# Optimization experiments

Measured on AMD Instinct MI355X. Metric: run time of the kernel, lower is better.

Reference implementation:

```python
import jax, jax.numpy as jnp
import numpy as np

VISION_TOKEN_TYPE = 1
HIDDEN = 4096
INTER = 11008


def setup_inputs() -> dict:
    key = jax.random.key(0)
    ks = jax.random.split(key, 8)
    B, L, D, F = 2, 2048, HIDDEN, INTER
    s_in = 1.0 / np.sqrt(D)
    s_mid = 1.0 / np.sqrt(F)
    inp = {
        "hidden_states": jax.random.normal(ks[0], (B, L, D), dtype=jnp.float32),
        "token_type_ids": jax.random.randint(ks[1], (B, L), 0, 2, dtype=jnp.int64),
        # language expert weights (stored as [in, out] for x @ W)
        "lang_gate": jax.random.normal(ks[2], (D, F), dtype=jnp.float32) * s_in,
        "lang_up": jax.random.normal(ks[3], (D, F), dtype=jnp.float32) * s_in,
        "lang_down": jax.random.normal(ks[4], (F, D), dtype=jnp.float32) * s_mid,
        # vision expert weights
        "vis_gate": jax.random.normal(ks[5], (D, F), dtype=jnp.float32) * s_in,
        "vis_up": jax.random.normal(ks[6], (D, F), dtype=jnp.float32) * s_in,
        "vis_down": jax.random.normal(ks[7], (F, D), dtype=jnp.float32) * s_mid,
    }
    return inp


def _swiglu_mlp(x, w_gate, w_up, w_down):
    # x: (B, L, D) -> (B, L, D)
    return (jax.nn.silu(x @ w_gate) * (x @ w_up)) @ w_down


def _vision_mask(token_type_ids):
    # vision token i is one whose type AND next token's type are VISION_TOKEN_TYPE;
    # last position is always language.
    is_vis = token_type_ids == VISION_TOKEN_TYPE
    pair = is_vis[:, :-1] & is_vis[:, 1:]
    return jnp.pad(pair, ((0, 0), (0, 1)), constant_values=False)  # (B, L) bool


def reference(hidden_states, token_type_ids, lang_gate, lang_up, lang_down,
              vis_gate, vis_up, vis_down):
    vision_mask = _vision_mask(token_type_ids)  # (B, L)
    out_vis = _swiglu_mlp(hidden_states, vis_gate, vis_up, vis_down)
    out_lang = _swiglu_mlp(hidden_states, lang_gate, lang_up, lang_down)
    return jnp.where(vision_mask[..., None], out_vis, out_lang)
```

## Files before the change

### kernel.cpp

```cpp
#include <hip/hip_runtime.h>
#include <cstdint>

#define HD 4096
#define FF 11008
#define BB 2
#define LL 2048
#define BL (BB*LL)
#define NM 16
#define NN 86

using bf16x8  = __attribute__((ext_vector_type(8))) __bf16;
using f32x4   = __attribute__((ext_vector_type(4))) float;
using ushort8 = __attribute__((ext_vector_type(8))) unsigned short;

__device__ __forceinline__ int imin(int a, int b) { return a < b ? a : b; }

__device__ __forceinline__ unsigned short f2bf(float f) {
  union { float f; unsigned u; } v; v.f = f;
  unsigned r = v.u + 0x7fffu + ((v.u >> 16) & 1u);
  return (unsigned short)(r >> 16);
}

__device__ __forceinline__ void gld_lds16(const void* g, void* l) {
  __builtin_amdgcn_global_load_lds(
      (__attribute__((address_space(1))) void*)g,
      (__attribute__((address_space(3))) void*)l, 16, 0, 0);
}

__global__ void detect_mode(const int* __restrict__ w, int* __restrict__ flag) {
  int acc = 0;
  for (int i = 1 + 2 * (int)threadIdx.x; i < BL; i += 512) acc |= w[i];
  if (acc != 0) atomicOr(flag, 1);
}

__global__ void mask_compact(const int* __restrict__ w, const int* __restrict__ flag,
                             int* __restrict__ cnts, int* __restrict__ idxL,
                             int* __restrict__ idxV) {
  int i = blockIdx.x * 256 + threadIdx.x;
  if (i >= BL) return;
  int p = i & (LL - 1);
  bool i32 = (*flag != 0);
  int ti = i32 ? w[i] : w[2 * i];
  bool vis = false;
  if (p < LL - 1) {
    int tn = i32 ? w[i + 1] : w[2 * (i + 1)];
    vis = (ti == 1) && (tn == 1);
  }
  if (vis) idxV[atomicAdd(&cnts[1], 1)] = i;
  else     idxL[atomicAdd(&cnts[0], 1)] = i;
}

__global__ void convx(const float* __restrict__ x, unsigned short* __restrict__ xb) {
  size_t i = ((size_t)blockIdx.x * 256 + threadIdx.x) * 8;
  float4 a = *(const float4*)(x + i);
  float4 b = *(const float4*)(x + i + 4);
  ushort8 o;
  o[0] = f2bf(a.x); o[1] = f2bf(a.y); o[2] = f2bf(a.z); o[3] = f2bf(a.w);
  o[4] = f2bf(b.x); o[5] = f2bf(b.y); o[6] = f2bf(b.z); o[7] = f2bf(b.w);
  *(ushort8*)(xb + i) = o;
}

__global__ void convT(const float* __restrict__ in, unsigned short* __restrict__ out,
                      int K, int N, int toff) {
  __shared__ unsigned short T[64][65];
  int n0 = blockIdx.x * 64, k0 = blockIdx.y * 64;
  int t = threadIdx.x;
  int cg = (t & 15) * 4;
  int r0 = t >> 4;
#pragma unroll
  for (int it = 0; it < 4; ++it) {
    int r = r0 + it * 16;
    float4 v = *(const float4*)(in + (size_t)(k0 + r) * N + n0 + cg);
    T[cg + 0][r] = f2bf(v.x); T[cg + 1][r] = f2bf(v.y);
    T[cg + 2][r] = f2bf(v.z); T[cg + 3][r] = f2bf(v.w);
  }
  __syncthreads();
  int nl = t >> 3, kg = t & 7;
#pragma unroll
  for (int it = 0; it < 2; ++it) {
    int n = nl + it * 32;
    ushort8 o;
#pragma unroll
    for (int j = 0; j < 8; ++j) o[j] = T[n][kg * 8 + j];
    int gn = n0 + n;
    size_t r = (toff < 0) ? (size_t)gn
                          : (size_t)(((gn >> 4) << 5) + toff + (gn & 15));
    *(ushort8*)(out + r * K + k0 + kg * 8) = o;
  }
}

#define BAR()  __builtin_amdgcn_s_barrier()
#define VMC(n) asm volatile("s_waitcnt vmcnt(" #n ")" ::: "memory")
#define LGK0() asm volatile("s_waitcnt lgkmcnt(0)" ::: "memory")

#define STG_A(h, kt) { \
  gld_lds16(aptr[h][0] + (kt) * 64, &lds[(((kt) & 1) << 14) + ((h) << 13) + w * 512]); \
  gld_lds16(aptr[h][1] + (kt) * 64, &lds[(((kt) & 1) << 14) + ((h) << 13) + (w + 8) * 512]); }
#define STG_B(h, kt) { \
  gld_lds16(bptr[h][0] + (kt) * 64, &lds[32768 + (((kt) & 1) << 14) + ((h) << 13) + w * 512]); \
  gld_lds16(bptr[h][1] + (kt) * 64, &lds[32768 + (((kt) & 1) << 14) + ((h) << 13) + (w + 8) * 512]); }

#define RD_A(s, rh) { _Pragma("unroll") \
  for (int mi = 0; mi < 4; ++mi) { \
    a[mi][0] = *(const bf16x8*)&lds[((s) << 14) + addrA[rh][mi]]; \
    a[mi][1] = *(const bf16x8*)&lds[((s) << 14) + (addrA[rh][mi] ^ 32)]; } }
#define RD_B(s, ch, br) { _Pragma("unroll") \
  for (int ni = 0; ni < 2; ++ni) { \
    br[ni][0] = *(const bf16x8*)&lds[((s) << 14) + addrB[ch][ni]]; \
    br[ni][1] = *(const bf16x8*)&lds[((s) << 14) + (addrB[ch][ni] ^ 32)]; } }

#define MFMA_Q(rh, br, ch) { \
  __builtin_amdgcn_s_setprio(1); \
  _Pragma("unroll") for (int mi = 0; mi < 4; ++mi) \
  _Pragma("unroll") for (int ni = 0; ni < 2; ++ni) { \
    acc[(rh)*4+mi][(ch)*2+ni] = __builtin_amdgcn_mfma_f32_16x16x32_bf16(a[mi][0], br[ni][0], acc[(rh)*4+mi][(ch)*2+ni], 0, 0, 0); \
    acc[(rh)*4+mi][(ch)*2+ni] = __builtin_amdgcn_mfma_f32_16x16x32_bf16(a[mi][1], br[ni][1], acc[(rh)*4+mi][(ch)*2+ni], 0, 0, 0); } \
  __builtin_amdgcn_s_setprio(0); }

__global__ __launch_bounds__(512, 2) void gemm1_8ph(
    const unsigned short* __restrict__ Xb, const unsigned short* __restrict__ Wgu,
    const int* __restrict__ idx, const int* __restrict__ cntp,
    unsigned short* __restrict__ H) {
  const int orig = blockIdx.x;
  const int xcd = orig & 7;
  const int pos = orig >> 3;
  const int wgid = xcd * (NM * NN / 8) + pos;
  const int bx = wgid >> 4;
  const int m0 = (wgid & 15) << 8;
  const int cnt = *cntp;
  if (cnt == 0 || m0 >= cnt) return;

  __shared__ __align__(16) unsigned short lds[65536];

  const int t = threadIdx.x, l = t & 63, w = t >> 6;
  const int wr = w >> 2, wc = w & 3;
  const int srcswz = (((l & 7) ^ (l >> 3)) << 3);

  const unsigned short* aptr[2][2];
  const unsigned short* bptr[2][2];
#pragma unroll
  for (int h = 0; h < 2; ++h)
#pragma unroll
    for (int j = 0; j < 2; ++j) {
      int r = h * 128 + (w + j * 8) * 8 + (l >> 3);
      int tok = idx[imin(m0 + r, cnt - 1)];
      aptr[h][j] = Xb + (size_t)tok * HD + srcswz;
      bptr[h][j] = Wgu + (size_t)(bx * 256 + r) * HD + srcswz;
    }

  const int koff0 = (((l >> 4) ^ (l & 7)) << 3);
  int addrA[2][4], addrB[2][2];
#pragma unroll
  for (int rh = 0; rh < 2; ++rh)
#pragma unroll
    for (int mi = 0; mi < 4; ++mi)
      addrA[rh][mi] = (wr * 128 + rh * 64 + mi * 16 + (l & 15)) * 64 + koff0;
#pragma unroll
  for (int ch = 0; ch < 2; ++ch)
#pragma unroll
    for (int ni = 0; ni < 2; ++ni)
      addrB[ch][ni] = 32768 + (wc * 64 + ch * 32 + ni * 16 + (l & 15)) * 64 + koff0;

  f32x4 acc[8][4] = {};
  bf16x8 a[4][2], b0[2][2], b1[2][2];

  STG_A(0, 0); STG_A(1, 0); STG_B(0, 0); STG_B(1, 0);
  STG_B(0, 1); STG_B(1, 1);
  VMC(4); BAR();

  const int NI = HD / 128;
  for (int i = 0; i < NI - 1; ++i) {
    const int kt1 = 2 * i + 1, kt2 = 2 * i + 2, kt3 = 2 * i + 3;
    RD_A(0, 0); RD_B(0, 0, b0); STG_A(0, kt1); BAR(); LGK0();
    MFMA_Q(0, b0, 0); BAR();
    RD_B(0, 1, b1); STG_A(1, kt1); BAR(); LGK0();
    MFMA_Q(0, b1, 1); BAR();
    RD_A(0, 1); STG_B(0, kt2); BAR(); LGK0();
    MFMA_Q(1, b0, 0); BAR();
    STG_B(1, kt2); VMC(4); BAR();
    MFMA_Q(1, b1, 1); BAR();
    RD_A(1, 0); RD_B(1, 0, b0); STG_A(0, kt2); BAR(); LGK0();
    MFMA_Q(0, b0, 0); BAR();
    RD_B(1, 1, b1); STG_A(1, kt2); BAR(); LGK0();
    MFMA_Q(0, b1, 1); BAR();
    RD_A(1, 1); STG_B(0, kt3); BAR(); LGK0();
    MFMA_Q(1, b0, 0); BAR();
    STG_B(1, kt3); VMC(4); BAR();
    MFMA_Q(1, b1, 1); BAR();
  }
  {
    const int kt1 = HD / 64 - 1;
    RD_A(0, 0); RD_B(0, 0, b0); STG_A(0, kt1); BAR(); LGK0();
    MFMA_Q(0, b0, 0); BAR();
    RD_B(0, 1, b1); STG_A(1, kt1); BAR(); LGK0();
    MFMA_Q(0, b1, 1); BAR();
    RD_A(0, 1); BAR(); LGK0();
    MFMA_Q(1, b0, 0); BAR();
    VMC(0); BAR();
    MFMA_Q(1, b1, 1); BAR();
    RD_A(1, 0); RD_B(1, 0, b0); BAR(); LGK0();
    MFMA_Q(0, b0, 0); BAR();
    RD_B(1, 1, b1); BAR(); LGK0();
    MFMA_Q(0, b1, 1); BAR();
    RD_A(1, 1); BAR(); LGK0();
    MFMA_Q(1, b0, 0); BAR();
    BAR();
    MFMA_Q(1, b1, 1); BAR();
  }

#pragma unroll
  for (int mi = 0; mi < 8; ++mi)
#pragma unroll
    for (int j = 0; j < 4; ++j) {
      int grow = m0 + wr * 128 + mi * 16 + ((l >> 4) << 2) + j;
      if (grow < cnt) {
        int token = idx[grow];
#pragma unroll
        for (int pair = 0; pair < 2; ++pair) {
          float g = acc[mi][pair * 2][j];
          float u = acc[mi][pair * 2 + 1][j];
          float h = (g / (1.f + __expf(-g))) * u;
          int f = bx * 128 + wc * 32 + pair * 16 + (l & 15);
          H[(size_t)token * FF + f] = f2bf(h);
        }
      }
    }
}

__global__ __launch_bounds__(256) void gemm2(
    const unsigned short* __restrict__ Hh, const unsigned short* __restrict__ Wd,
    const int* __restrict__ idx, const int* __restrict__ cntp,
    float* __restrict__ Out) {
  const int cnt = *cntp;
  const int m0 = blockIdx.y * 128;
  if (cnt == 0 || m0 >= cnt) return;
  const int n0 = blockIdx.x * 128;

  __shared__ __align__(16) unsigned short sA[128 * 64];
  __shared__ __align__(16) unsigned short sB[128 * 64];

  const int t = threadIdx.x, l = t & 63, w = t >> 6;
  const int wr = w >> 1, wc = w & 1;
  const int c = l & 7, lr = l >> 3;
  const int choff = ((c ^ lr) << 3);

  int tokA[4];
#pragma unroll
  for (int i = 0; i < 4; ++i)
    tokA[i] = idx[imin(m0 + (w * 4 + i) * 8 + lr, cnt - 1)];

  int offA[2][4], offB[2][4];
#pragma unroll
  for (int kk = 0; kk < 2; ++kk) {
#pragma unroll
    for (int mi = 0; mi < 4; ++mi) {
      int m = wr * 64 + mi * 16 + (l & 15);
      offA[kk][mi] = m * 64 + ((((kk << 2) + (l >> 4)) ^ (m & 7)) << 3);
    }
#pragma unroll
    for (int ni = 0; ni < 4; ++ni) {
      int n = wc * 64 + ni * 16 + (l & 15);
      offB[kk][ni] = n * 64 + ((((kk << 2) + (l >> 4)) ^ (n & 7)) << 3);
    }
  }

  f32x4 acc[4][4] = {};

  for (int k0 = 0; k0 < FF; k0 += 64) {
#pragma unroll
    for (int i = 0; i < 4; ++i)
      gld_lds16(Hh + (size_t)tokA[i] * FF + k0 + choff, &sA[(w * 4 + i) * 512]);
#pragma unroll
    for (int i = 0; i < 4; ++i) {
      int n = (w * 4 + i) * 8 + lr;
      gld_lds16(Wd + (size_t)(n0 + n) * FF + k0 + choff, &sB[(w * 4 + i) * 512]);
    }
    __syncthreads();
#pragma unroll
    for (int kk = 0; kk < 2; ++kk) {
      bf16x8 a[4], b[4];
#pragma unroll
      for (int mi = 0; mi < 4; ++mi) a[mi] = *(const bf16x8*)&sA[offA[kk][mi]];
#pragma unroll
      for (int ni = 0; ni < 4; ++ni) b[ni] = *(const bf16x8*)&sB[offB[kk][ni]];
#pragma unroll
      for (int mi = 0; mi < 4; ++mi)
#pragma unroll
        for (int ni = 0; ni < 4; ++ni)
          acc[mi][ni] = __builtin_amdgcn_mfma_f32_16x16x32_bf16(a[mi], b[ni], acc[mi][ni], 0, 0, 0);
    }
    __syncthreads();
  }

#pragma unroll
  for (int mi = 0; mi < 4; ++mi)
#pragma unroll
    for (int j = 0; j < 4; ++j) {
      int grow = m0 + wr * 64 + mi * 16 + ((l >> 4) << 2) + j;
      if (grow < cnt) {
        int token = idx[grow];
        size_t base = (size_t)token * HD + n0 + wc * 64 + (l & 15);
#pragma unroll
        for (int ni = 0; ni < 4; ++ni)
          Out[base + ni * 16] = acc[mi][ni][j];
      }
    }
}

extern "C" void kernel_launch(void* const* d_in, const int* in_sizes, int n_in,
                              void* d_out, int out_size, void* d_ws, size_t ws_size,
                              hipStream_t stream) {
  const float* hs = (const float*)d_in[0];
  const int*   tt = (const int*)d_in[1];
  const float* lg = (const float*)d_in[2];
  const float* lu = (const float*)d_in[3];
  const float* ld = (const float*)d_in[4];
  const float* vg = (const float*)d_in[5];
  const float* vu = (const float*)d_in[6];
  const float* vd = (const float*)d_in[7];
  float* out = (float*)d_out;
  char* ws = (char*)d_ws;

  int* cnts = (int*)ws;
  int* flag = (int*)(ws + 8);
  int* idxL = (int*)(ws + 1024);
  int* idxV = (int*)(ws + 1024 + BL * 4);
  unsigned short* Xb  = (unsigned short*)(ws + 65536);
  unsigned short* Hb  = Xb + (size_t)BL * HD;
  unsigned short* Wgu = Hb + (size_t)BL * FF;

  hipMemsetAsync(ws, 0, 64, stream);
  detect_mode<<<1, 256, 0, stream>>>(tt, flag);
  mask_compact<<<BL / 256, 256, 0, stream>>>(tt, flag, cnts, idxL, idxV);
  convx<<<(BL * HD / 8) / 256, 256, 0, stream>>>(hs, Xb);

  convT<<<dim3(FF / 64, HD / 64), 256, 0, stream>>>(lg, Wgu, HD, FF, 0);
  convT<<<dim3(FF / 64, HD / 64), 256, 0, stream>>>(lu, Wgu, HD, FF, 16);
  gemm1_8ph<<<dim3(NM * NN), 512, 0, stream>>>(Xb, Wgu, idxL, cnts + 0, Hb);
  convT<<<dim3(FF / 64, HD / 64), 256, 0, stream>>>(vg, Wgu, HD, FF, 0);
  convT<<<dim3(FF / 64, HD / 64), 256, 0, stream>>>(vu, Wgu, HD, FF, 16);
  gemm1_8ph<<<dim3(NM * NN), 512, 0, stream>>>(Xb, Wgu, idxV, cnts + 1, Hb);

  convT<<<dim3(HD / 64, FF / 64), 256, 0, stream>>>(ld, Wgu, FF, HD, -1);
  gemm2<<<dim3(HD / 128, BL / 128), 256, 0, stream>>>(Hb, Wgu, idxL, cnts + 0, out);
  convT<<<dim3(HD / 64, FF / 64), 256, 0, stream>>>(vd, Wgu, FF, HD, -1);
  gemm2<<<dim3(HD / 128, BL / 128), 256, 0, stream>>>(Hb, Wgu, idxV, cnts + 1, out);
}
```

Measured before the change: 1.685 ms.

## Replace gemm2 with 256x256 8-phase pipelined kernel fusing both experts

Rewrites the down-projection GEMM to reuse the 512-thread, 256x256-tile, 8-phase LDS-pipelined main loop from gemm1 (factored into a macro). Both the language and vision experts now run in a single launch, with the M-block index split between the two token lists. The two down weights are transposed into separate workspace buffers so one kernel can read both. The aim is higher MFMA utilisation and better data reuse than the simple 128x128 double-sync kernel, plus less launch and tail overhead. The cost is more workspace use and a larger register/LDS footprint per block.

Result: no change. 1.700 ms (+0.8%).

```diff
diff --git a/kernel.cpp b/kernel.cpp
--- a/kernel.cpp
+++ b/kernel.cpp
@@ -8,6 +8,7 @@
 #define BL (BB*LL)
 #define NM 16
 #define NN 86
+#define MB2 17
 
 using bf16x8  = __attribute__((ext_vector_type(8))) __bf16;
 using f32x4   = __attribute__((ext_vector_type(4))) float;
@@ -94,11 +95,11 @@
 #define LGK0() asm volatile("s_waitcnt lgkmcnt(0)" ::: "memory")
 
 #define STG_A(h, kt) { \
-  gld_lds16(aptr[h][0] + (kt) * 64, &lds[(((kt) & 1) << 14) + ((h) << 13) + w * 512]); \
-  gld_lds16(aptr[h][1] + (kt) * 64, &lds[(((kt) & 1) << 14) + ((h) << 13) + (w + 8) * 512]); }
+  gld_lds16(aptr[h][0] + (size_t)(kt) * 64, &lds[(((kt) & 1) << 14) + ((h) << 13) + w * 512]); \
+  gld_lds16(aptr[h][1] + (size_t)(kt) * 64, &lds[(((kt) & 1) << 14) + ((h) << 13) + (w + 8) * 512]); }
 #define STG_B(h, kt) { \
-  gld_lds16(bptr[h][0] + (kt) * 64, &lds[32768 + (((kt) & 1) << 14) + ((h) << 13) + w * 512]); \
-  gld_lds16(bptr[h][1] + (kt) * 64, &lds[32768 + (((kt) & 1) << 14) + ((h) << 13) + (w + 8) * 512]); }
+  gld_lds16(bptr[h][0] + (size_t)(kt) * 64, &lds[32768 + (((kt) & 1) << 14) + ((h) << 13) + w * 512]); \
+  gld_lds16(bptr[h][1] + (size_t)(kt) * 64, &lds[32768 + (((kt) & 1) << 14) + ((h) << 13) + (w + 8) * 512]); }
 
 #define RD_A(s, rh) { _Pragma("unroll") \
   for (int mi = 0; mi < 4; ++mi) { \
@@ -116,6 +117,49 @@
     acc[(rh)*4+mi][(ch)*2+ni] = __builtin_amdgcn_mfma_f32_16x16x32_bf16(a[mi][0], br[ni][0], acc[(rh)*4+mi][(ch)*2+ni], 0, 0, 0); \
     acc[(rh)*4+mi][(ch)*2+ni] = __builtin_amdgcn_mfma_f32_16x16x32_bf16(a[mi][1], br[ni][1], acc[(rh)*4+mi][(ch)*2+ni], 0, 0, 0); } \
   __builtin_amdgcn_s_setprio(0); }
+
+#define KLOOP_8PH(KEXT) \
+  STG_A(0, 0); STG_A(1, 0); STG_B(0, 0); STG_B(1, 0); \
+  STG_B(0, 1); STG_B(1, 1); \
+  VMC(4); BAR(); \
+  for (int i = 0; i < (KEXT) / 128 - 1; ++i) { \
+    const int kt1 = 2 * i + 1, kt2 = 2 * i + 2, kt3 = 2 * i + 3; \
+    RD_A(0, 0); RD_B(0, 0, b0); STG_A(0, kt1); BAR(); LGK0(); \
+    MFMA_Q(0, b0, 0); BAR(); \
+    RD_B(0, 1, b1); STG_A(1, kt1); BAR(); LGK0(); \
+    MFMA_Q(0, b1, 1); BAR(); \
+    RD_A(0, 1); STG_B(0, kt2); BAR(); LGK0(); \
+    MFMA_Q(1, b0, 0); BAR(); \
+    STG_B(1, kt2); VMC(4); BAR(); \
+    MFMA_Q(1, b1, 1); BAR(); \
+    RD_A(1, 0); RD_B(1, 0, b0); STG_A(0, kt2); BAR(); LGK0(); \
+    MFMA_Q(0, b0, 0); BAR(); \
+    RD_B(1, 1, b1); STG_A(1, kt2); BAR(); LGK0(); \
+    MFMA_Q(0, b1, 1); BAR(); \
+    RD_A(1, 1); STG_B(0, kt3); BAR(); LGK0(); \
+    MFMA_Q(1, b0, 0); BAR(); \
+    STG_B(1, kt3); VMC(4); BAR(); \
+    MFMA_Q(1, b1, 1); BAR(); \
+  } \
+  { \
+    const int kt1 = (KEXT) / 64 - 1; \
+    RD_A(0, 0); RD_B(0, 0, b0); STG_A(0, kt1); BAR(); LGK0(); \
+    MFMA_Q(0, b0, 0); BAR(); \
+    RD_B(0, 1, b1); STG_A(1, kt1); BAR(); LGK0(); \
+    MFMA_Q(0, b1, 1); BAR(); \
+    RD_A(0, 1); BAR(); LGK0(); \
+    MFMA_Q(1, b0, 0); BAR(); \
+    VMC(0); BAR(); \
+    MFMA_Q(1, b1, 1); BAR(); \
+    RD_A(1, 0); RD_B(1, 0, b0); BAR(); LGK0(); \
+    MFMA_Q(0, b0, 0); BAR(); \
+    RD_B(1, 1, b1); BAR(); LGK0(); \
+    MFMA_Q(0, b1, 1); BAR(); \
+    RD_A(1, 1); BAR(); LGK0(); \
+    MFMA_Q(1, b0, 0); BAR(); \
+    BAR(); \
+    MFMA_Q(1, b1, 1); BAR(); \
+  }
 
 __global__ __launch_bounds__(512, 2) void gemm1_8ph(
     const unsigned short* __restrict__ Xb, const unsigned short* __restrict__ Wgu,
@@ -164,49 +208,7 @@
   f32x4 acc[8][4] = {};
   bf16x8 a[4][2], b0[2][2], b1[2][2];
 
-  STG_A(0, 0); STG_A(1, 0); STG_B(0, 0); STG_B(1, 0);
-  STG_B(0, 1); STG_B(1, 1);
-  VMC(4); BAR();
-
-  const int NI = HD / 128;
-  for (int i = 0; i < NI - 1; ++i) {
-    const int kt1 = 2 * i + 1, kt2 = 2 * i + 2, kt3 = 2 * i + 3;
-    RD_A(0, 0); RD_B(0, 0, b0); STG_A(0, kt1); BAR(); LGK0();
-    MFMA_Q(0, b0, 0); BAR();
-    RD_B(0, 1, b1); STG_A(1, kt1); BAR(); LGK0();
-    MFMA_Q(0, b1, 1); BAR();
-    RD_A(0, 1); STG_B(0, kt2); BAR(); LGK0();
-    MFMA_Q(1, b0, 0); BAR();
-    STG_B(1, kt2); VMC(4); BAR();
-    MFMA_Q(1, b1, 1); BAR();
-    RD_A(1, 0); RD_B(1, 0, b0); STG_A(0, kt2); BAR(); LGK0();
-    MFMA_Q(0, b0, 0); BAR();
-    RD_B(1, 1, b1); STG_A(1, kt2); BAR(); LGK0();
-    MFMA_Q(0, b1, 1); BAR();
-    RD_A(1, 1); STG_B(0, kt3); BAR(); LGK0();
-    MFMA_Q(1, b0, 0); BAR();
-    STG_B(1, kt3); VMC(4); BAR();
-    MFMA_Q(1, b1, 1); BAR();
-  }
-  {
-    const int kt1 = HD / 64 - 1;
-    RD_A(0, 0); RD_B(0, 0, b0); STG_A(0, kt1); BAR(); LGK0();
-    MFMA_Q(0, b0, 0); BAR();
-    RD_B(0, 1, b1); STG_A(1, kt1); BAR(); LGK0();
-    MFMA_Q(0, b1, 1); BAR();
-    RD_A(0, 1); BAR(); LGK0();
-    MFMA_Q(1, b0, 0); BAR();
-    VMC(0); BAR();
-    MFMA_Q(1, b1, 1); BAR();
-    RD_A(1, 0); RD_B(1, 0, b0); BAR(); LGK0();
-    MFMA_Q(0, b0, 0); BAR();
-    RD_B(1, 1, b1); BAR(); LGK0();
-    MFMA_Q(0, b1, 1); BAR();
-    RD_A(1, 1); BAR(); LGK0();
-    MFMA_Q(1, b0, 0); BAR();
-    BAR();
-    MFMA_Q(1, b1, 1); BAR();
-  }
+  KLOOP_8PH(HD)
 
 #pragma unroll
   for (int mi = 0; mi < 8; ++mi)
@@ -227,82 +229,72 @@
     }
 }
 
-__global__ __launch_bounds__(256) void gemm2(
-    const unsigned short* __restrict__ Hh, const unsigned short* __restrict__ Wd,
-    const int* __restrict__ idx, const int* __restrict__ cntp,
-    float* __restrict__ Out) {
-  const int cnt = *cntp;
-  const int m0 = blockIdx.y * 128;
-  if (cnt == 0 || m0 >= cnt) return;
-  const int n0 = blockIdx.x * 128;
-
-  __shared__ __align__(16) unsigned short sA[128 * 64];
-  __shared__ __align__(16) unsigned short sB[128 * 64];
+__global__ __launch_bounds__(512, 2) void gemm2_8ph(
+    const unsigned short* __restrict__ Hh,
+    const unsigned short* __restrict__ Wd0, const unsigned short* __restrict__ Wd1,
+    const int* __restrict__ idxL, const int* __restrict__ idxV,
+    const int* __restrict__ cnts, float* __restrict__ Out) {
+  const int wg = blockIdx.x;
+  const int bx = wg / MB2;
+  int mb = wg - bx * MB2;
+  const int cntL = cnts[0], cntV = cnts[1];
+  const int nL = (cntL + 255) >> 8;
+  const int* idx; const unsigned short* Wd; int cnt;
+  if (mb < nL) { idx = idxL; Wd = Wd0; cnt = cntL; }
+  else {
+    mb -= nL;
+    if (mb >= ((cntV + 255) >> 8)) return;
+    idx = idxV; Wd = Wd1; cnt = cntV;
+  }
+  const int m0 = mb << 8;
+
+  __shared__ __align__(16) unsigned short lds[65536];
 
   const int t = threadIdx.x, l = t & 63, w = t >> 6;
-  const int wr = w >> 1, wc = w & 1;
-  const int c = l & 7, lr = l >> 3;
-  const int choff = ((c ^ lr) << 3);
-
-  int tokA[4];
-#pragma unroll
-  for (int i = 0; i < 4; ++i)
-    tokA[i] = idx[imin(m0 + (w * 4 + i) * 8 + lr, cnt - 1)];
-
-  int offA[2][4], offB[2][4];
-#pragma unroll
-  for (int kk = 0; kk < 2; ++kk) {
-#pragma unroll
-    for (int mi = 0; mi < 4; ++mi) {
-      int m = wr * 64 + mi * 16 + (l & 15);
-      offA[kk][mi] = m * 64 + ((((kk << 2) + (l >> 4)) ^ (m & 7)) << 3);
+  const int wr = w >> 2, wc = w & 3;
+  const int srcswz = (((l & 7) ^ (l >> 3)) << 3);
+
+  const unsigned short* aptr[2][2];
+  const unsigned short* bptr[2][2];
+#pragma unroll
+  for (int h = 0; h < 2; ++h)
+#pragma unroll
+    for (int j = 0; j < 2; ++j) {
+      int r = h * 128 + (w + j * 8) * 8 + (l >> 3);
+      int tok = idx[imin(m0 + r, cnt - 1)];
+      aptr[h][j] = Hh + (size_t)tok * FF + srcswz;
+      bptr[h][j] = Wd + (size_t)(bx * 256 + r) * FF + srcswz;
     }
-#pragma unroll
-    for (int ni = 0; ni < 4; ++ni) {
-      int n = wc * 64 + ni * 16 + (l & 15);
-      offB[kk][ni] = n * 64 + ((((kk << 2) + (l >> 4)) ^ (n & 7)) << 3);
-    }
-  }
-
-  f32x4 acc[4][4] = {};
-
-  for (int k0 = 0; k0 < FF; k0 += 64) {
-#pragma unroll
-    for (int i = 0; i < 4; ++i)
-      gld_lds16(Hh + (size_t)tokA[i] * FF + k0 + choff, &sA[(w * 4 + i) * 512]);
-#pragma unroll
-    for (int i = 0; i < 4; ++i) {
-      int n = (w * 4 + i) * 8 + lr;
-      gld_lds16(Wd + (size_t)(n0 + n) * FF + k0 + choff, &sB[(w * 4 + i) * 512]);
-    }
-    __syncthreads();
-#pragma unroll
-    for (int kk = 0; kk < 2; ++kk) {
-      bf16x8 a[4], b[4];
-#pragma unroll
-      for (int mi = 0; mi < 4; ++mi) a[mi] = *(const bf16x8*)&sA[offA[kk][mi]];
-#pragma unroll
-      for (int ni = 0; ni < 4; ++ni) b[ni] = *(const bf16x8*)&sB[offB[kk][ni]];
-#pragma unroll
-      for (int mi = 0; mi < 4; ++mi)
-#pragma unroll
-        for (int ni = 0; ni < 4; ++ni)
-          acc[mi][ni] = __builtin_amdgcn_mfma_f32_16x16x32_bf16(a[mi], b[ni], acc[mi][ni], 0, 0, 0);
-    }
-    __syncthreads();
-  }
-
-#pragma unroll
-  for (int mi = 0; mi < 4; ++mi)
+
+  const int koff0 = (((l >> 4) ^ (l & 7)) << 3);
+  int addrA[2][4], addrB[2][2];
+#pragma unroll
+  for (int rh = 0; rh < 2; ++rh)
+#pragma unroll
+    for (int mi = 0; mi < 4; ++mi)
+      addrA[rh][mi] = (wr * 128 + rh * 64 + mi * 16 + (l & 15)) * 64 + koff0;
+#pragma unroll
+  for (int ch = 0; ch < 2; ++ch)
+#pragma unroll
+    for (int ni = 0; ni < 2; ++ni)
+      addrB[ch][ni] = 32768 + (wc * 64 + ch * 32 + ni * 16 + (l & 15)) * 64 + koff0;
+
+  f32x4 acc[8][4] = {};
+  bf16x8 a[4][2], b0[2][2], b1[2][2];
+
+  KLOOP_8PH(FF)
+
+#pragma unroll
+  for (int mi = 0; mi < 8; ++mi)
 #pragma unroll
     for (int j = 0; j < 4; ++j) {
-      int grow = m0 + wr * 64 + mi * 16 + ((l >> 4) << 2) + j;
+      int grow = m0 + wr * 128 + mi * 16 + ((l >> 4) << 2) + j;
       if (grow < cnt) {
         int token = idx[grow];
-        size_t base = (size_t)token * HD + n0 + wc * 64 + (l & 15);
-#pragma unroll
-        for (int ni = 0; ni < 4; ++ni)
-          Out[base + ni * 16] = acc[mi][ni][j];
+        size_t base = (size_t)token * HD + bx * 256 + wc * 64 + (l & 15);
+#pragma unroll
+        for (int nf = 0; nf < 4; ++nf)
+          Out[base + nf * 16] = acc[mi][nf][j];
       }
     }
 }
@@ -328,6 +320,8 @@
   unsigned short* Xb  = (unsigned short*)(ws + 65536);
   unsigned short* Hb  = Xb + (size_t)BL * HD;
   unsigned short* Wgu = Hb + (size_t)BL * FF;
+  unsigned short* Wd0 = Wgu;
+  unsigned short* Wd1 = Wgu + (size_t)HD * FF;
 
   hipMemsetAsync(ws, 0, 64, stream);
   detect_mode<<<1, 256, 0, stream>>>(tt, flag);
@@ -341,8 +335,7 @@
   convT<<<dim3(FF / 64, HD / 64), 256, 0, stream>>>(vu, Wgu, HD, FF, 16);
   gemm1_8ph<<<dim3(NM * NN), 512, 0, stream>>>(Xb, Wgu, idxV, cnts + 1, Hb);
 
-  convT<<<dim3(HD / 64, FF / 64), 256, 0, stream>>>(ld, Wgu, FF, HD, -1);
-  gemm2<<<dim3(HD / 128, BL / 128), 256, 0, stream>>>(Hb, Wgu, idxL, cnts + 0, out);
-  convT<<<dim3(HD / 64, FF / 64), 256, 0, stream>>>(vd, Wgu, FF, HD, -1);
-  gemm2<<<dim3(HD / 128, BL / 128), 256, 0, stream>>>(Hb, Wgu, idxV, cnts + 1, out);
-}
+  convT<<<dim3(HD / 64, FF / 64), 256, 0, stream>>>(ld, Wd0, FF, HD, -1);
+  convT<<<dim3(HD / 64, FF / 64), 256, 0, stream>>>(vd, Wd1, FF, HD, -1);
+  gemm2_8ph<<<dim3((HD / 256) * MB2), 512, 0, stream>>>(Hb, Wd0, Wd1, idxL, idxV, cnts, out);
+}
```
